# Kernel tuning notes

Measured on AMD Instinct MI355X. Metric: run time of the kernel, lower is better.

## Reference

```python
import jax, jax.numpy as jnp
import numpy as np

NNK = 16
DENSITY_WEIGHT = 1.0


def _sq_dist(x, y):
    # x: [B, Nx, C], y: [B, Ny, C] -> [B, Nx, Ny] squared L2 distances.
    # Matmul form of the original broadcast-diff computation (same math,
    # avoids materializing [B, Nx, C, Ny]); clamp tiny negatives from fp error.
    x2 = jnp.sum(x * x, axis=-1)               # [B, Nx]
    y2 = jnp.sum(y * y, axis=-1)               # [B, Ny]
    xy = jnp.einsum('bnc,bmc->bnm', x, y)      # [B, Nx, Ny]
    return jnp.maximum(x2[:, :, None] + y2[:, None, :] - 2.0 * xy, 0.0)


def _safe_sqrt(s):
    # sqrt with zero (instead of inf) gradient at s == 0; forward values exact.
    pos = s > 0
    return jnp.where(pos, jnp.sqrt(jnp.where(pos, s, 1.0)), 0.0)


def setup_inputs() -> dict:
    key = jax.random.key(0)
    k1, k2 = jax.random.split(key)
    B, N, C = 2, 8192, 3
    y_pred = jax.random.normal(k1, (B, N, C), dtype=jnp.float32)
    y_true = jax.random.normal(k2, (B, N, C), dtype=jnp.float32)
    return {"y_pred": y_pred, "y_true": y_true}


def reference(y_pred, y_true):
    # dist[b, i, j] = || y_true[b, i] - y_pred[b, j] ||
    dist = _safe_sqrt(_sq_dist(y_true, y_pred))            # [B, Nt, Np]
    minrow = jnp.min(dist, axis=2)                         # per true point
    mincol = jnp.min(dist, axis=1)                         # per pred point
    shape_loss = (jnp.mean(minrow) + jnp.mean(mincol)) / 2

    dist2 = _safe_sqrt(_sq_dist(y_true, y_true))           # [B, Nt, Nt]
    knndis, _ = jax.lax.top_k(-dist, NNK)                  # [B, Nt, k]
    knndis2, _ = jax.lax.top_k(-dist2, NNK)                # [B, Nt, k]
    density_loss = jnp.mean(jnp.abs(knndis - knndis2))

    data_loss = shape_loss + density_loss * DENSITY_WEIGHT
    return (data_loss, shape_loss, density_loss)
```

## Files before the change

### kernel.cpp

```cpp
#include <hip/hip_runtime.h>
#include <math.h>

#define NPTS 8192
#define NB 2
#define NROWS (NB * NPTS)
#define KNN 16
#define KC 6

#define GRID 32
#define NCELLS (GRID * GRID * GRID)
#define TOTCELLS (4 * NCELLS)
#define H 0.35f
#define RLO (-5.6f)
#define INVH (1.0f / H)
#define SCAN_BLOCKS 128
#define SEGCAP 132

#define QC 3
#define WLCAP 49152
#define QBLOCKS 2048

__device__ __forceinline__ int cellof(float x) {
  int c = (int)floorf((x - RLO) * INVH);
  return min(max(c, 0), GRID - 1);
}

__device__ __forceinline__ float sqd3(float qx, float qy, float qz, float4 c) {
  float dx = qx - c.x, dy = qy - c.y, dz = qz - c.z;
  return fmaf(dx, dx, fmaf(dy, dy, dz * dz));
}

__device__ __forceinline__ int lanerank(unsigned long long mk) {
  return __builtin_amdgcn_mbcnt_hi((unsigned)(mk >> 32),
                                   __builtin_amdgcn_mbcnt_lo((unsigned)mk, 0));
}

template <int K>
__device__ __forceinline__ void insertK(float (&a)[K], float d) {
  if (d < a[K - 1]) {
    a[K - 1] = d;
#pragma unroll
    for (int k = K - 1; k > 0; --k) {
      float lo = fminf(a[k - 1], a[k]);
      a[k] = fmaxf(a[k - 1], a[k]);
      a[k - 1] = lo;
    }
  }
}

__device__ __forceinline__ float bitonic_sort64(float v, int lane) {
#pragma unroll
  for (int k = 2; k <= 64; k <<= 1) {
#pragma unroll
    for (int j = k >> 1; j >= 1; j >>= 1) {
      float o = __shfl_xor(v, j, 64);
      bool up = ((lane & k) == 0);
      bool lower = ((lane & j) == 0);
      float mn = fminf(v, o), mx = fmaxf(v, o);
      v = (up == lower) ? mn : mx;
    }
  }
  return v;
}

template <int K, int NEEDQ>
__device__ __forceinline__ void wave_grid_knn_q(
    int g, int cx, int cy, int cz,
    const float (&qx)[QC], const float (&qy)[QC], const float (&qz)[QC],
    const float4* __restrict__ sorted, const unsigned* __restrict__ pack,
    unsigned* sS, unsigned* sC, unsigned* sPre, int lane,
    float (&a)[QC][K], float (&dminq)[QC], int (&cntq)[QC],
    float (&bnd2q)[QC]) {
  float fq[QC];
#pragma unroll
  for (int q = 0; q < QC; ++q) {
    float fx = fminf(qx[q] - (RLO + cx * H), (RLO + (cx + 1) * H) - qx[q]);
    float fy = fminf(qy[q] - (RLO + cy * H), (RLO + (cy + 1) * H) - qy[q]);
    float fz = fminf(qz[q] - (RLO + cz * H), (RLO + (cz + 1) * H) - qz[q]);
    fq[q] = fminf(fx, fminf(fy, fz));
  }
  const int base = g * NCELLS;
  for (int m = 0; m <= GRID; ++m) {
    const int zlo = max(cz - m, 0), zhi = min(cz + m, GRID - 1);
    const int ylo = max(cy - m, 0), yhi = min(cy + m, GRID - 1);
    const int xlo = max(cx - m, 0), xhi = min(cx + m, GRID - 1);
    const int ny = yhi - ylo + 1;
    const int nrows = (zhi - zlo + 1) * ny;
    for (int rb = 0; rb < nrows; rb += 64) {
      const int rho = rb + lane;
      const bool act = rho < nrows;
      const int rr = act ? rho : 0;
      const int z = zlo + rr / ny, y = ylo + rr % ny;
      const int dza = abs(z - cz), dya = abs(y - cy);
      const bool bdry = (dza == m) || (dya == m);
      unsigned stA = 0, cnA = 0, stB = 0, cnB = 0;
      const int rowbase = base + (z * GRID + y) * GRID;
      if (act) {
        if (bdry) {
          unsigned plo = pack[rowbase + xlo];
          unsigned phi = pack[rowbase + xhi];
          stA = plo >> 14;
          cnA = ((phi >> 14) + (phi & 16383u)) - stA;
        } else {
          int xl = cx - m, xr = cx + m;
          if (xl >= 0) { unsigned p = pack[rowbase + xl]; stA = p >> 14; cnA = p & 16383u; }
          if (xr < GRID) { unsigned p = pack[rowbase + xr]; stB = p >> 14; cnB = p & 16383u; }
        }
      }
      unsigned long long mA = __ballot(cnA > 0);
      unsigned long long mB = __ballot(cnB > 0);
      int nA = __popcll(mA);
      int nseg = nA + __popcll(mB);
      if (nseg == 0) continue;
      int slA = lanerank(mA), slB = nA + lanerank(mB);
      if (cnA > 0) { sS[slA] = stA; sC[slA] = cnA; }
      if (cnB > 0) { sS[slB] = stB; sC[slB] = cnB; }
      unsigned total = 0;
      for (int h = 0; h < 2; ++h) {
        int sl = h * 64 + lane;
        unsigned v = (sl < nseg) ? sC[sl] : 0u;
        unsigned inc = v;
#pragma unroll
        for (int s2 = 1; s2 < 64; s2 <<= 1) {
          unsigned t = __shfl_up(inc, s2, 64);
          if (lane >= s2) inc += t;
        }
        if (sl < nseg) sPre[sl] = total + inc - v;
        total += __shfl(inc, 63, 64);
        if (nseg <= 64) break;
      }
      int sh0 = (nseg > 1) ? (1 << (31 - __clz(nseg - 1))) : 0;
      for (unsigned cb = 0; cb < total; cb += 64) {
        unsigned c = cb + (unsigned)lane;
        bool cact = c < total;
        unsigned cc = cact ? c : (total - 1);
        int lo = 0;
        for (int sh = sh0; sh; sh >>= 1) {
          int mid = lo + sh;
          if (mid < nseg && sPre[mid] <= cc) lo = mid;
        }
        float4 p = sorted[sS[lo] + (cc - sPre[lo])];
#pragma unroll
        for (int q = 0; q < QC; ++q) {
          float d = cact ? sqd3(qx[q], qy[q], qz[q], p) : INFINITY;
          dminq[q] = fminf(dminq[q], fmaxf(d, a[q][K - 1]));
          insertK(a[q], d);
        }
      }
    }
#pragma unroll
    for (int q = 0; q < QC; ++q) {
      float bnd = fmaxf((float)m * H + fq[q], 0.0f) * 0.999f;
      bnd2q[q] = bnd * bnd;
    }
    int cpA = 0, cpB = 0;
#pragma unroll
    for (int k = 0; k < K; ++k) {
      cpA += (a[0][k] <= bnd2q[0] ? 1 : 0) + (a[1][k] <= bnd2q[1] ? 65536 : 0);
      cpB += (a[2][k] <= bnd2q[2] ? 1 : 0);
    }
#pragma unroll
    for (int s2 = 1; s2 < 64; s2 <<= 1) {
      cpA += __shfl_xor(cpA, s2, 64);
      cpB += __shfl_xor(cpB, s2, 64);
    }
    cntq[0] = cpA & 0xffff;
    cntq[1] = cpA >> 16;
    cntq[2] = cpB;
    bool okall = (cntq[0] >= NEEDQ) && (cntq[1] >= NEEDQ) && (cntq[2] >= NEEDQ);
    bool covered = (zlo == 0 && zhi == GRID - 1 && ylo == 0 && yhi == GRID - 1 &&
                    xlo == 0 && xhi == GRID - 1);
    if (okall || covered) break;
  }
}

__global__ __launch_bounds__(256) void count_kernel(
    const float* __restrict__ yp, const float* __restrict__ yt,
    unsigned* __restrict__ counts, int* __restrict__ pflat,
    unsigned* __restrict__ prank, unsigned* __restrict__ wcnt) {
  if (blockIdx.x == 0 && threadIdx.x < 8) wcnt[threadIdx.x] = 0;
  int t = blockIdx.x * 256 + threadIdx.x;
  const float* src;
  int g;
  if (t < NROWS) { src = yp + 3 * t; g = 2 * (t >> 13); }
  else { int u = t - NROWS; src = yt + 3 * u; g = 2 * (u >> 13) + 1; }
  int flat = g * NCELLS + (cellof(src[2]) * GRID + cellof(src[1])) * GRID + cellof(src[0]);
  unsigned r = atomicAdd(&counts[flat], 1u);
  pflat[t] = flat;
  prank[t] = r;
}

__global__ __launch_bounds__(1024) void scan1_kernel(
    const unsigned* __restrict__ counts, unsigned* __restrict__ partial,
    unsigned* __restrict__ aux) {
  __shared__ unsigned ws[16];
  const int t = threadIdx.x, lane = t & 63, wave = t >> 6;
  const int tid = blockIdx.x * 1024 + t;
  unsigned v = counts[tid];
  unsigned inc = v;
#pragma unroll
  for (int off = 1; off < 64; off <<= 1) {
    unsigned u = __shfl_up(inc, off, 64);
    if (lane >= off) inc += u;
  }
  if (lane == 63) ws[wave] = inc;
  __syncthreads();
  unsigned wex = 0;
  if (wave == 0) {
    unsigned o = (lane < 16) ? ws[lane] : 0u;
    unsigned wi = o;
#pragma unroll
    for (int off = 1; off < 16; off <<= 1) {
      unsigned u = __shfl_up(wi, off, 64);
      if (lane >= off) wi += u;
    }
    if (lane < 16) ws[lane] = wi - o;
  }
  __syncthreads();
  wex = ws[wave];
  partial[tid] = wex + inc - v;
  if (t == 1023) aux[blockIdx.x] = wex + inc;
}

__global__ __launch_bounds__(1024) void pack_kernel(
    const unsigned* __restrict__ counts, const unsigned* __restrict__ partial,
    const unsigned* __restrict__ aux, unsigned* __restrict__ pack,
    unsigned* __restrict__ wcnt, unsigned* __restrict__ wlist) {
  __shared__ unsigned sa[2];
  const int t = threadIdx.x;
  if (t < 128) {
    unsigned v = (t < (int)blockIdx.x) ? aux[t] : 0u;
#pragma unroll
    for (int s = 1; s < 64; s <<= 1) v += __shfl_xor(v, s, 64);
    if ((t & 63) == 0) sa[t >> 6] = v;
  }
  __syncthreads();
  unsigned base = sa[0] + sa[1];
  int i = blockIdx.x * 1024 + t;
  unsigned cnti = counts[i];
  pack[i] = ((partial[i] + base) << 14) | cnti;
  if (cnti > 0) {
    int g = i >> 15;
    unsigned b = (unsigned)(g >> 1);
    unsigned cellw = (unsigned)(i & (NCELLS - 1));
    unsigned nch = (cnti + QC - 1) / QC;
    if (g & 1) {
      unsigned slot = atomicAdd(&wcnt[4], 2 * nch);
      for (unsigned j = 0; j < nch; ++j) {
        wlist[slot + 2 * j]     = (b << 30) | (0u << 28) | (cellw << 13) | j;
        wlist[slot + 2 * j + 1] = (b << 30) | (1u << 28) | (cellw << 13) | j;
      }
    } else {
      unsigned slot = atomicAdd(&wcnt[4], nch);
      for (unsigned j = 0; j < nch; ++j)
        wlist[slot + j] = (b << 30) | (2u << 28) | (cellw << 13) | j;
    }
  }
}

__global__ __launch_bounds__(256) void scatter_kernel(
    const float* __restrict__ yp, const float* __restrict__ yt,
    const unsigned* __restrict__ pack, const int* __restrict__ pflat,
    const unsigned* __restrict__ prank, float4* __restrict__ sorted) {
  int t = blockIdx.x * 256 + threadIdx.x;
  const float* src;
  int row;
  if (t < NROWS) { row = t; src = yp + 3 * t; }
  else { row = t - NROWS; src = yt + 3 * row; }
  unsigned pos = (pack[pflat[t]] >> 14) + prank[t];
  sorted[pos] = make_float4(src[0], src[1], src[2], __int_as_float(row));
}

__global__ __launch_bounds__(256) void query_kernel(
    const float4* __restrict__ sorted, const unsigned* __restrict__ pack,
    const unsigned* __restrict__ wcnt, const unsigned* __restrict__ wlist,
    float* __restrict__ knnP, float* __restrict__ knnT,
    float* __restrict__ mincol_arr, unsigned* __restrict__ flags) {
  __shared__ unsigned sb[4][3][SEGCAP];
  __shared__ float cbw[4][64];
  const int wave = threadIdx.x >> 6, lane = threadIdx.x & 63;
  unsigned* sS = sb[wave][0];
  unsigned* sC = sb[wave][1];
  unsigned* sP = sb[wave][2];
  float* cbuf = cbw[wave];
  const unsigned nwork = wcnt[4];
  const unsigned nw = gridDim.x * 4;
  for (unsigned wrk = blockIdx.x * 4 + wave; wrk < nwork; wrk += nw) {
    const unsigned e = wlist[wrk];
    const int b = (int)((e >> 30) & 1u);
    const int task = (int)((e >> 28) & 3u);
    const int cell = (int)((e >> 13) & 32767u);
    const int qoff = (int)(e & 8191u) * QC;
    const int qg = (task == 2) ? 2 * b : 2 * b + 1;
    const int tg = (task == 0) ? 2 * b : 2 * b + 1;
    const unsigned pc = pack[qg * NCELLS + cell];
    const int cstart = (int)(pc >> 14);
    const int ccnt = (int)(pc & 16383u);
    const int nq = min(QC, ccnt - qoff);
    const int cx = cell & (GRID - 1), cy = (cell >> 5) & (GRID - 1), cz = cell >> 10;

    float qx[QC], qy[QC], qz[QC];
    int rowq[QC];
#pragma unroll
    for (int q = 0; q < QC; ++q) {
      float4 eq = sorted[cstart + qoff + min(q, nq - 1)];
      qx[q] = eq.x; qy[q] = eq.y; qz[q] = eq.z;
      rowq[q] = __float_as_int(eq.w);
    }

    if (task < 2) {
      float a[QC][KC];
      float dminq[QC];
#pragma unroll
      for (int q = 0; q < QC; ++q) {
        dminq[q] = INFINITY;
#pragma unroll
        for (int k = 0; k < KC; ++k) a[q][k] = INFINITY;
      }
      int cntq[QC];
      float bnd2q[QC];
      wave_grid_knn_q<KC, KNN>(tg, cx, cy, cz, qx, qy, qz, sorted, pack,
                               sS, sC, sP, lane, a, dminq, cntq, bnd2q);
      float* dstbase = (task == 0) ? knnP : knnT;
#pragma unroll
      for (int q = 0; q < QC; ++q) {
        if (q >= nq) break;
        float tau;
        if (cntq[q] >= KNN && cntq[q] <= 64) {
          tau = bnd2q[q];
        } else {
          float slm = bitonic_sort64(a[q][0], lane);
          tau = __shfl(slm, 15, 64);
        }
        int tot = 0;
        int idxk[KC];
#pragma unroll
        for (int k = 0; k < KC; ++k) {
          unsigned long long mk = __ballot(a[q][k] <= tau);
          idxk[k] = tot + lanerank(mk);
          tot += __popcll(mk);
        }
#pragma unroll
        for (int k = 0; k < KC; ++k)
          if (a[q][k] <= tau && idxk[k] < 64) cbuf[idxk[k]] = a[q][k];
        float v = (lane < tot) ? cbuf[lane] : INFINITY;
        v = bitonic_sort64(v, lane);
        float f15 = __shfl(v, 15, 64);
        bool bad = (tot > 64) || (__ballot(dminq[q] <= f15) != 0ull);
        if (lane < KNN) dstbase[rowq[q] * KNN + lane] = sqrtf(v);
        if (lane == 0) flags[task * NROWS + rowq[q]] = bad ? 1u : 0u;
      }
    } else {
      float a1[QC][1];
      float dminq[QC];
#pragma unroll
      for (int q = 0; q < QC; ++q) { a1[q][0] = INFINITY; dminq[q] = INFINITY; }
      int cntq[QC];
      float bnd2q[QC];
      wave_grid_knn_q<1, 1>(tg, cx, cy, cz, qx, qy, qz, sorted, pack,
                            sS, sC, sP, lane, a1, dminq, cntq, bnd2q);
#pragma unroll
      for (int q = 0; q < QC; ++q) {
        if (q >= nq) break;
        float v = a1[q][0];
#pragma unroll
        for (int s2 = 1; s2 < 64; s2 <<= 1) v = fminf(v, __shfl_xor(v, s2, 64));
        if (lane == 0) mincol_arr[rowq[q]] = sqrtf(v);
      }
    }
  }
}

__device__ float exact16_rowlist(const float4* __restrict__ base,
                                 float qx, float qy, float qz, int lane) {
  float a[KNN];
#pragma unroll
  for (int k = 0; k < KNN; ++k) a[k] = INFINITY;
  for (int s = 0; s < NPTS / 64; ++s) {
    float d = sqd3(qx, qy, qz, base[s * 64 + lane]);
    insertK(a, d);
  }
  float res = INFINITY;
#pragma unroll 1
  for (int r = 0; r < KNN; ++r) {
    float v = a[0];
    int idx = lane;
#pragma unroll
    for (int s = 1; s < 64; s <<= 1) {
      float ov = __shfl_xor(v, s, 64);
      int oi = __shfl_xor(idx, s, 64);
      bool take = (ov < v) || (ov == v && oi < idx);
      v = take ? ov : v;
      idx = take ? oi : idx;
    }
    if (lane == r) res = v;
    if (lane == idx) {
#pragma unroll
      for (int k = 0; k < KNN - 1; ++k) a[k] = a[k + 1];
      a[KNN - 1] = INFINITY;
    }
  }
  return res;
}

__global__ __launch_bounds__(256) void combine_kernel(
    const float* __restrict__ yt, const float4* __restrict__ sorted,
    const unsigned* __restrict__ flags, float* __restrict__ knnP,
    float* __restrict__ knnT, const float* __restrict__ mincol_arr,
    double* __restrict__ pd) {
  __shared__ double s1[256], s2[256], s3[256];
  const int t = threadIdx.x, lane = t & 63, wave = t >> 6;
  const int row0 = blockIdx.x * 256;
  const int rbase = row0 + wave * 64;
  unsigned f0 = flags[rbase + lane];
  unsigned f1 = flags[NROWS + rbase + lane];
  unsigned long long m0 = __ballot(f0 != 0u);
  unsigned long long m1 = __ballot(f1 != 0u);
  while (m0) {
    int rr = __ffsll(m0) - 1; m0 &= m0 - 1;
    int row = rbase + rr;
    int bb = row >> 13;
    const float* q = yt + 3 * row;
    float s = exact16_rowlist(sorted + (size_t)(2 * bb) * NPTS, q[0], q[1], q[2], lane);
    if (lane < KNN) knnP[row * KNN + lane] = sqrtf(s);
  }
  while (m1) {
    int rr = __ffsll(m1) - 1; m1 &= m1 - 1;
    int row = rbase + rr;
    int bb = row >> 13;
    const float* q = yt + 3 * row;
    float s = exact16_rowlist(sorted + (size_t)(2 * bb + 1) * NPTS, q[0], q[1], q[2], lane);
    if (lane < KNN) knnT[row * KNN + lane] = sqrtf(s);
  }
  __syncthreads();
  const int row = row0 + t;
  float s = 0.0f;
#pragma unroll
  for (int k = 0; k < KNN; ++k)
    s += fabsf(knnP[row * KNN + k] - knnT[row * KNN + k]);
  s1[t] = (double)knnP[row * KNN];
  s2[t] = (double)mincol_arr[row];
  s3[t] = (double)s;
  __syncthreads();
  for (int off = 128; off > 0; off >>= 1) {
    if (t < off) { s1[t] += s1[t + off]; s2[t] += s2[t + off]; s3[t] += s3[t + off]; }
    __syncthreads();
  }
  if (t == 0) {
    pd[blockIdx.x * 3 + 0] = s1[0];
    pd[blockIdx.x * 3 + 1] = s2[0];
    pd[blockIdx.x * 3 + 2] = s3[0];
  }
}

__global__ __launch_bounds__(64) void finalize_kernel(
    const double* __restrict__ pd, float* __restrict__ out) {
  const int t = threadIdx.x;
  double a = pd[t * 3], b = pd[t * 3 + 1], c = pd[t * 3 + 2];
#pragma unroll
  for (int s = 32; s >= 1; s >>= 1) {
    a += __shfl_down(a, s, 64);
    b += __shfl_down(b, s, 64);
    c += __shfl_down(c, s, 64);
  }
  if (t == 0) {
    double shape = 0.5 * (a + b) / (double)NROWS;
    double dens = c / ((double)NROWS * KNN);
    out[0] = (float)(shape + dens);
    out[1] = (float)shape;
    out[2] = (float)dens;
  }
}

extern "C" void kernel_launch(void* const* d_in, const int* in_sizes, int n_in,
                              void* d_out, int out_size, void* d_ws, size_t ws_size,
                              hipStream_t stream) {
  (void)in_sizes; (void)n_in; (void)out_size; (void)ws_size;
  const float* yp = (const float*)d_in[0];
  const float* yt = (const float*)d_in[1];
  char* w = (char*)d_ws;
  unsigned* counts  = (unsigned*)w;  w += TOTCELLS * 4;
  unsigned* partial = (unsigned*)w;  w += TOTCELLS * 4;
  unsigned* aux     = (unsigned*)w;  w += 512;
  unsigned* pack    = (unsigned*)w;  w += TOTCELLS * 4;
  int*      pflat   = (int*)w;       w += 2 * NROWS * 4;
  unsigned* prank   = (unsigned*)w;  w += 2 * NROWS * 4;
  float4*   sorted  = (float4*)w;    w += 2 * NROWS * 16;
  float*    knnP    = (float*)w;     w += NROWS * KNN * 4;
  float*    knnT    = (float*)w;     w += NROWS * KNN * 4;
  float*    mincol  = (float*)w;     w += NROWS * 4;
  unsigned* flags   = (unsigned*)w;  w += 2 * NROWS * 4;
  double*   pd      = (double*)w;    w += 64 * 3 * 8;
  unsigned* wcnt    = (unsigned*)w;  w += 64;
  unsigned* wlist   = (unsigned*)w;  w += WLCAP * 4;
  float* out = (float*)d_out;

  hipMemsetAsync(counts, 0, (size_t)TOTCELLS * 4, stream);
  count_kernel<<<2 * NROWS / 256, 256, 0, stream>>>(yp, yt, counts, pflat, prank, wcnt);
  scan1_kernel<<<SCAN_BLOCKS, 1024, 0, stream>>>(counts, partial, aux);
  pack_kernel<<<SCAN_BLOCKS, 1024, 0, stream>>>(counts, partial, aux, pack, wcnt, wlist);
  scatter_kernel<<<2 * NROWS / 256, 256, 0, stream>>>(yp, yt, pack, pflat, prank, sorted);
  query_kernel<<<QBLOCKS, 256, 0, stream>>>(sorted, pack, wcnt, wlist,
                                            knnP, knnT, mincol, flags);
  combine_kernel<<<64, 256, 0, stream>>>(yt, sorted, flags, knnP, knnT, mincol, pd);
  finalize_kernel<<<1, 64, 0, stream>>>(pd, out);
}
```

Baseline: 154.5 us.

## Fuse pred/true kNN tasks per query, reduce in-kernel, use atomic work queue

```diff
diff --git a/kernel.cpp b/kernel.cpp
--- a/kernel.cpp
+++ b/kernel.cpp
@@ -174,11 +174,40 @@
   }
 }
 
+template <int K>
+__device__ __forceinline__ float epilogue16(float (&aq)[K], float dmin,
+                                            int cnt, float bnd2, float* cbuf,
+                                            int lane, bool& bad) {
+  float tau;
+  if (cnt >= KNN && cnt <= 64) {
+    tau = bnd2;
+  } else {
+    float slm = bitonic_sort64(aq[0], lane);
+    tau = __shfl(slm, 15, 64);
+  }
+  int tot = 0;
+  int idxk[K];
+#pragma unroll
+  for (int k = 0; k < K; ++k) {
+    unsigned long long mk = __ballot(aq[k] <= tau);
+    idxk[k] = tot + lanerank(mk);
+    tot += __popcll(mk);
+  }
+#pragma unroll
+  for (int k = 0; k < K; ++k)
+    if (aq[k] <= tau && idxk[k] < 64) cbuf[idxk[k]] = aq[k];
+  float v = (lane < tot) ? cbuf[lane] : INFINITY;
+  v = bitonic_sort64(v, lane);
+  float f15 = __shfl(v, 15, 64);
+  bad = (tot > 64) || (__ballot(dmin <= f15) != 0ull);
+  return v;
+}
+
 __global__ __launch_bounds__(256) void count_kernel(
     const float* __restrict__ yp, const float* __restrict__ yt,
     unsigned* __restrict__ counts, int* __restrict__ pflat,
     unsigned* __restrict__ prank, unsigned* __restrict__ wcnt) {
-  if (blockIdx.x == 0 && threadIdx.x < 8) wcnt[threadIdx.x] = 0;
+  if (blockIdx.x == 0 && threadIdx.x < 16) wcnt[threadIdx.x] = 0;
   int t = blockIdx.x * 256 + threadIdx.x;
   const float* src;
   int g;
@@ -244,17 +273,10 @@
     unsigned b = (unsigned)(g >> 1);
     unsigned cellw = (unsigned)(i & (NCELLS - 1));
     unsigned nch = (cnti + QC - 1) / QC;
-    if (g & 1) {
-      unsigned slot = atomicAdd(&wcnt[4], 2 * nch);
-      for (unsigned j = 0; j < nch; ++j) {
-        wlist[slot + 2 * j]     = (b << 30) | (0u << 28) | (cellw << 13) | j;
-        wlist[slot + 2 * j + 1] = (b << 30) | (1u << 28) | (cellw << 13) | j;
-      }
-    } else {
-      unsigned slot = atomicAdd(&wcnt[4], nch);
-      for (unsigned j = 0; j < nch; ++j)
-        wlist[slot + j] = (b << 30) | (2u << 28) | (cellw << 13) | j;
-    }
+    unsigned task = (g & 1) ? 0u : 2u;
+    unsigned slot = atomicAdd(&wcnt[4], nch);
+    for (unsigned j = 0; j < nch; ++j)
+      wlist[slot + j] = (b << 30) | (task << 28) | (cellw << 13) | j;
   }
 }
 
@@ -273,26 +295,29 @@
 
 __global__ __launch_bounds__(256) void query_kernel(
     const float4* __restrict__ sorted, const unsigned* __restrict__ pack,
-    const unsigned* __restrict__ wcnt, const unsigned* __restrict__ wlist,
-    float* __restrict__ knnP, float* __restrict__ knnT,
+    unsigned* __restrict__ wcnt, const unsigned* __restrict__ wlist,
+    float* __restrict__ minrow_arr, float* __restrict__ densrow,
     float* __restrict__ mincol_arr, unsigned* __restrict__ flags) {
   __shared__ unsigned sb[4][3][SEGCAP];
   __shared__ float cbw[4][64];
+  __shared__ float vPw[4][QC][16];
   const int wave = threadIdx.x >> 6, lane = threadIdx.x & 63;
   unsigned* sS = sb[wave][0];
   unsigned* sC = sb[wave][1];
   unsigned* sP = sb[wave][2];
   float* cbuf = cbw[wave];
   const unsigned nwork = wcnt[4];
-  const unsigned nw = gridDim.x * 4;
-  for (unsigned wrk = blockIdx.x * 4 + wave; wrk < nwork; wrk += nw) {
+  for (;;) {
+    unsigned wrk;
+    if (lane == 0) wrk = atomicAdd(&wcnt[5], 1u);
+    wrk = (unsigned)__shfl((int)wrk, 0, 64);
+    if (wrk >= nwork) break;
     const unsigned e = wlist[wrk];
     const int b = (int)((e >> 30) & 1u);
     const int task = (int)((e >> 28) & 3u);
     const int cell = (int)((e >> 13) & 32767u);
     const int qoff = (int)(e & 8191u) * QC;
     const int qg = (task == 2) ? 2 * b : 2 * b + 1;
-    const int tg = (task == 0) ? 2 * b : 2 * b + 1;
     const unsigned pc = pack[qg * NCELLS + cell];
     const int cstart = (int)(pc >> 14);
     const int ccnt = (int)(pc & 16383u);
@@ -308,56 +333,60 @@
       rowq[q] = __float_as_int(eq.w);
     }
 
-    if (task < 2) {
+    if (task == 0) {
       float a[QC][KC];
       float dminq[QC];
+      int cntq[QC];
+      float bnd2q[QC];
+      unsigned badbits = 0;
 #pragma unroll
       for (int q = 0; q < QC; ++q) {
         dminq[q] = INFINITY;
 #pragma unroll
         for (int k = 0; k < KC; ++k) a[q][k] = INFINITY;
       }
-      int cntq[QC];
-      float bnd2q[QC];
-      wave_grid_knn_q<KC, KNN>(tg, cx, cy, cz, qx, qy, qz, sorted, pack,
+      wave_grid_knn_q<KC, KNN>(2 * b, cx, cy, cz, qx, qy, qz, sorted, pack,
                                sS, sC, sP, lane, a, dminq, cntq, bnd2q);
-      float* dstbase = (task == 0) ? knnP : knnT;
 #pragma unroll
       for (int q = 0; q < QC; ++q) {
         if (q >= nq) break;
-        float tau;
-        if (cntq[q] >= KNN && cntq[q] <= 64) {
-          tau = bnd2q[q];
-        } else {
-          float slm = bitonic_sort64(a[q][0], lane);
-          tau = __shfl(slm, 15, 64);
+        bool bad;
+        float v = epilogue16(a[q], dminq[q], cntq[q], bnd2q[q], cbuf, lane, bad);
+        if (lane < KNN) vPw[wave][q][lane] = sqrtf(v);
+        if (bad) badbits |= (1u << q);
+      }
+#pragma unroll
+      for (int q = 0; q < QC; ++q) {
+        dminq[q] = INFINITY;
+#pragma unroll
+        for (int k = 0; k < KC; ++k) a[q][k] = INFINITY;
+      }
+      wave_grid_knn_q<KC, KNN>(2 * b + 1, cx, cy, cz, qx, qy, qz, sorted, pack,
+                               sS, sC, sP, lane, a, dminq, cntq, bnd2q);
+#pragma unroll
+      for (int q = 0; q < QC; ++q) {
+        if (q >= nq) break;
+        bool bad;
+        float v = epilogue16(a[q], dminq[q], cntq[q], bnd2q[q], cbuf, lane, bad);
+        float vp = (lane < KNN) ? vPw[wave][q][lane] : 0.0f;
+        float d = (lane < KNN) ? fabsf(vp - sqrtf(v)) : 0.0f;
+#pragma unroll
+        for (int s2 = 1; s2 < 16; s2 <<= 1) d += __shfl_xor(d, s2, 64);
+        float mr = __shfl(vp, 0, 64);
+        if (lane == 0) {
+          minrow_arr[rowq[q]] = mr;
+          densrow[rowq[q]] = d;
+          flags[rowq[q]] = ((badbits >> q) & 1u) | bad ? 1u : 0u;
         }
-        int tot = 0;
-        int idxk[KC];
-#pragma unroll
-        for (int k = 0; k < KC; ++k) {
-          unsigned long long mk = __ballot(a[q][k] <= tau);
-          idxk[k] = tot + lanerank(mk);
-          tot += __popcll(mk);
-        }
-#pragma unroll
-        for (int k = 0; k < KC; ++k)
-          if (a[q][k] <= tau && idxk[k] < 64) cbuf[idxk[k]] = a[q][k];
-        float v = (lane < tot) ? cbuf[lane] : INFINITY;
-        v = bitonic_sort64(v, lane);
-        float f15 = __shfl(v, 15, 64);
-        bool bad = (tot > 64) || (__ballot(dminq[q] <= f15) != 0ull);
-        if (lane < KNN) dstbase[rowq[q] * KNN + lane] = sqrtf(v);
-        if (lane == 0) flags[task * NROWS + rowq[q]] = bad ? 1u : 0u;
       }
     } else {
       float a1[QC][1];
       float dminq[QC];
-#pragma unroll
-      for (int q = 0; q < QC; ++q) { a1[q][0] = INFINITY; dminq[q] = INFINITY; }
       int cntq[QC];
       float bnd2q[QC];
-      wave_grid_knn_q<1, 1>(tg, cx, cy, cz, qx, qy, qz, sorted, pack,
+#pragma unroll
+      for (int q = 0; q < QC; ++q) { a1[q][0] = INFINITY; dminq[q] = INFINITY; }
+      wave_grid_knn_q<1, 1>(2 * b + 1, cx, cy, cz, qx, qy, qz, sorted, pack,
                             sS, sC, sP, lane, a1, dminq, cntq, bnd2q);
 #pragma unroll
       for (int q = 0; q < QC; ++q) {
@@ -405,42 +434,37 @@
 
 __global__ __launch_bounds__(256) void combine_kernel(
     const float* __restrict__ yt, const float4* __restrict__ sorted,
-    const unsigned* __restrict__ flags, float* __restrict__ knnP,
-    float* __restrict__ knnT, const float* __restrict__ mincol_arr,
+    const unsigned* __restrict__ flags, float* __restrict__ minrow_arr,
+    float* __restrict__ densrow, const float* __restrict__ mincol_arr,
     double* __restrict__ pd) {
   __shared__ double s1[256], s2[256], s3[256];
   const int t = threadIdx.x, lane = t & 63, wave = t >> 6;
   const int row0 = blockIdx.x * 256;
   const int rbase = row0 + wave * 64;
   unsigned f0 = flags[rbase + lane];
-  unsigned f1 = flags[NROWS + rbase + lane];
   unsigned long long m0 = __ballot(f0 != 0u);
-  unsigned long long m1 = __ballot(f1 != 0u);
   while (m0) {
     int rr = __ffsll(m0) - 1; m0 &= m0 - 1;
     int row = rbase + rr;
     int bb = row >> 13;
     const float* q = yt + 3 * row;
-    float s = exact16_rowlist(sorted + (size_t)(2 * bb) * NPTS, q[0], q[1], q[2], lane);
-    if (lane < KNN) knnP[row * KNN + lane] = sqrtf(s);
-  }
-  while (m1) {
-    int rr = __ffsll(m1) - 1; m1 &= m1 - 1;
-    int row = rbase + rr;
-    int bb = row >> 13;
-    const float* q = yt + 3 * row;
-    float s = exact16_rowlist(sorted + (size_t)(2 * bb + 1) * NPTS, q[0], q[1], q[2], lane);
-    if (lane < KNN) knnT[row * KNN + lane] = sqrtf(s);
+    float sPq = exact16_rowlist(sorted + (size_t)(2 * bb) * NPTS,
+                                q[0], q[1], q[2], lane);
+    float sTq = exact16_rowlist(sorted + (size_t)(2 * bb + 1) * NPTS,
+                                q[0], q[1], q[2], lane);
+    float vp = (lane < KNN) ? sqrtf(sPq) : 0.0f;
+    float vt = (lane < KNN) ? sqrtf(sTq) : 0.0f;
+    float d = fabsf(vp - vt);
+#pragma unroll
+    for (int s = 1; s < 16; s <<= 1) d += __shfl_xor(d, s, 64);
+    float mr = __shfl(vp, 0, 64);
+    if (lane == 0) { minrow_arr[row] = mr; densrow[row] = d; }
   }
   __syncthreads();
   const int row = row0 + t;
-  float s = 0.0f;
-#pragma unroll
-  for (int k = 0; k < KNN; ++k)
-    s += fabsf(knnP[row * KNN + k] - knnT[row * KNN + k]);
-  s1[t] = (double)knnP[row * KNN];
+  s1[t] = (double)minrow_arr[row];
   s2[t] = (double)mincol_arr[row];
-  s3[t] = (double)s;
+  s3[t] = (double)densrow[row];
   __syncthreads();
   for (int off = 128; off > 0; off >>= 1) {
     if (t < off) { s1[t] += s1[t + off]; s2[t] += s2[t + off]; s3[t] += s3[t + off]; }
@@ -486,10 +510,10 @@
   int*      pflat   = (int*)w;       w += 2 * NROWS * 4;
   unsigned* prank   = (unsigned*)w;  w += 2 * NROWS * 4;
   float4*   sorted  = (float4*)w;    w += 2 * NROWS * 16;
-  float*    knnP    = (float*)w;     w += NROWS * KNN * 4;
-  float*    knnT    = (float*)w;     w += NROWS * KNN * 4;
+  float*    minrow  = (float*)w;     w += NROWS * 4;
+  float*    densrow = (float*)w;     w += NROWS * 4;
   float*    mincol  = (float*)w;     w += NROWS * 4;
-  unsigned* flags   = (unsigned*)w;  w += 2 * NROWS * 4;
+  unsigned* flags   = (unsigned*)w;  w += NROWS * 4;
   double*   pd      = (double*)w;    w += 64 * 3 * 8;
   unsigned* wcnt    = (unsigned*)w;  w += 64;
   unsigned* wlist   = (unsigned*)w;  w += WLCAP * 4;
@@ -501,7 +525,8 @@
   pack_kernel<<<SCAN_BLOCKS, 1024, 0, stream>>>(counts, partial, aux, pack, wcnt, wlist);
   scatter_kernel<<<2 * NROWS / 256, 256, 0, stream>>>(yp, yt, pack, pflat, prank, sorted);
   query_kernel<<<QBLOCKS, 256, 0, stream>>>(sorted, pack, wcnt, wlist,
-                                            knnP, knnT, mincol, flags);
-  combine_kernel<<<64, 256, 0, stream>>>(yt, sorted, flags, knnP, knnT, mincol, pd);
+                                            minrow, densrow, mincol, flags);
+  combine_kernel<<<64, 256, 0, stream>>>(yt, sorted, flags, minrow, densrow,
+                                         mincol, pd);
   finalize_kernel<<<1, 64, 0, stream>>>(pd, out);
 }
```

Result: slower. 351.5 us (+127.5%).
